# Kernel tuning notes

Measured on AMD Instinct MI355X. Metric: run time of the kernel, lower is better.

## Reference

```python
import jax, jax.numpy as jnp
import numpy as np

SEQ_LEN = 256
INPUT_DIM = 1
HIDDEN = 2048
CLASSES = 10
BATCH = 128


def setup_inputs() -> dict:
    key = jax.random.key(0)
    ks = jax.random.split(key, 6)
    x = jax.random.normal(ks[0], (BATCH, SEQ_LEN), dtype=jnp.float32)
    # Gate order along the 4H axis: g (cell candidate), i, f, o.
    Wx = jax.random.normal(ks[1], (INPUT_DIM, 4 * HIDDEN), dtype=jnp.float32) * 0.1
    Wh = jax.random.normal(ks[2], (HIDDEN, 4 * HIDDEN), dtype=jnp.float32) * (1.0 / np.sqrt(HIDDEN))
    b = jax.random.normal(ks[3], (4 * HIDDEN,), dtype=jnp.float32) * 0.1
    Wph = jax.random.normal(ks[4], (HIDDEN, CLASSES), dtype=jnp.float32) * (1.0 / np.sqrt(HIDDEN))
    bp = jax.random.normal(ks[5], (CLASSES,), dtype=jnp.float32) * 0.1
    return {"x": x, "Wx": Wx, "Wh": Wh, "b": b, "Wph": Wph, "bp": bp}


def reference(x, Wx, Wh, b, Wph, bp):
    B, T = x.shape
    H = Wh.shape[0]
    # Original loops over seq_length - 1 timesteps.
    xs = x[:, : T - 1].T[:, :, None]  # [T-1, B, 1]

    def step(carry, x_t):
        h, c = carry
        z = x_t @ Wx + h @ Wh + b  # [B, 4H] fused gate GEMM
        g = jnp.tanh(z[:, 0 * H:1 * H])
        i = jax.nn.sigmoid(z[:, 1 * H:2 * H])
        f = jax.nn.sigmoid(z[:, 2 * H:3 * H])
        o = jax.nn.sigmoid(z[:, 3 * H:4 * H])
        c = g * i + c * f
        h = jnp.tanh(c) * o
        return (h, c), None

    h0 = jnp.zeros((B, H), dtype=x.dtype)
    c0 = jnp.zeros((B, H), dtype=x.dtype)
    (h, _), _ = jax.lax.scan(step, (h0, c0), xs)
    logits = h @ Wph + bp
    return jax.nn.softmax(logits, axis=1)
```

## Files before the change

kernel.cpp:

```cpp
#include <hip/hip_runtime.h>
#include <hip/hip_bf16.h>

#define SEQ_LEN 256
#define HIDDEN  2048
#define CLASSES 10
#define BATCH   128
#define NWG     256
#define WG_THREADS 512
#define STEPS   (SEQ_LEN - 1)
#define KTILES  64
#define PF      16
#define LDS_WH  131072
#define LDS_ALL (LDS_WH + 4096)

typedef __attribute__((ext_vector_type(8))) short  bf16x8;
typedef __attribute__((ext_vector_type(8))) unsigned short u16x8;
typedef __attribute__((ext_vector_type(4))) float  f32x4;
typedef __attribute__((ext_vector_type(4))) unsigned int u32x4;

#define WHP_OFF  0
#define HB_OFF   33554432UL
#define HF_OFF   (HB_OFF + 4UL * 524288UL)
#define BAR_OFF  (HF_OFF + 1048576UL)

__device__ __forceinline__ unsigned short f2bf(float f) {
    unsigned int u = __float_as_uint(f);
    return (unsigned short)((u + 0x7FFFu + ((u >> 16) & 1u)) >> 16);
}
__device__ __forceinline__ float sigm(float z)  { return 1.0f / (1.0f + __expf(-z)); }
__device__ __forceinline__ float tanh_f(float z){ return 2.0f / (1.0f + __expf(-2.0f * z)) - 1.0f; }

__device__ __forceinline__ unsigned int aload(const unsigned int* p) {
    return __hip_atomic_load(p, __ATOMIC_RELAXED, __HIP_MEMORY_SCOPE_AGENT);
}
__device__ __forceinline__ void astore(unsigned int* p, unsigned int v) {
    __hip_atomic_store(p, v, __ATOMIC_RELAXED, __HIP_MEMORY_SCOPE_AGENT);
}

__global__ void lstm_pack_kernel(const float* __restrict__ Wh,
                                 unsigned short* __restrict__ whp,
                                 unsigned short* __restrict__ hbufs,
                                 unsigned int* __restrict__ bar) {
    int chunk = blockIdx.x * 256 + threadIdx.x;
    int lane = chunk & 63;
    int nt   = (chunk >> 6) & 1;
    int kt   = (chunk >> 7) & 63;
    int W    = chunk >> 13;
    int q = lane >> 4, l16 = lane & 15;
    int c32  = nt * 16 + l16;
    int gate = c32 >> 3, u = c32 & 7;
    int n    = gate * 2048 + W * 8 + u;
    int k0   = kt * 32 + q * 8;
    u16x8 frag;
    #pragma unroll
    for (int j = 0; j < 8; ++j)
        frag[j] = f2bf(Wh[(size_t)(k0 + j) * 8192 + n]);
    ((u16x8*)whp)[chunk] = frag;

    if (chunk < 32768) ((u32x4*)hbufs)[chunk] = (u32x4){0, 0, 0, 0};
    if (chunk < 2048) bar[chunk] = 0u;
}

__device__ __forceinline__ void grid_barrier(unsigned int* bar, unsigned int phase,
                                             bool do_inv, int W) {
    __syncthreads();
    if (threadIdx.x < 64) {
        const int lane = threadIdx.x;
        if (lane == 0) astore(&bar[W], phase);
        if (W < 8) {
            unsigned int* sl = &bar[W * 32 + (lane & 31)];
            while (!__all((int)(aload(sl) >= phase)))
                __builtin_amdgcn_s_sleep(1);
            if (lane == 0) astore(&bar[512 + 16 * W], phase);
            if (W == 0) {
                unsigned int* dn = &bar[512 + 16 * (lane & 7)];
                while (!__all((int)(aload(dn) >= phase)))
                    __builtin_amdgcn_s_sleep(1);
                if (lane < 32) astore(&bar[1024 + 16 * lane], phase);
            }
        }
        if (lane == 0 && W != 0) {
            unsigned int* rl = &bar[1024 + 16 * (W & 31)];
            while (aload(rl) < phase)
                __builtin_amdgcn_s_sleep(1);
        }
        if (do_inv)
            __builtin_amdgcn_fence(__ATOMIC_ACQUIRE, "agent");
    }
    __syncthreads();
}

__global__ __launch_bounds__(WG_THREADS, 2) void lstm_persist(
    const float* __restrict__ x,  const float* __restrict__ Wx,
    const float* __restrict__ b,  const float* __restrict__ Wph,
    const float* __restrict__ bp, const unsigned short* __restrict__ whp,
    unsigned short* hbufs, float* hfin,
    unsigned int* bar, float* out)
{
    extern __shared__ char lds[];
    const int tid = threadIdx.x;
    const int W   = blockIdx.x;

    {
        const u32x4* src = (const u32x4*)whp + (size_t)W * 8192;
        u32x4* dst = (u32x4*)lds;
        for (int i = tid; i < 8192; i += WG_THREADS) dst[i] = src[i];
    }
    unsigned short* hstage = (unsigned short*)(lds + LDS_WH);
    __syncthreads();

    const int lane = tid & 63;
    const int wv   = tid >> 6;
    const int q    = lane >> 4;
    const int l16  = lane & 15;
    const int s    = (lane >> 3) & 1;
    const int u    = lane & 7;
    const int rowA = wv * 16 + l16;
    const int row0 = wv * 16 + q * 4;
    const int colh = W * 8 + u;

    const int n0 = ((l16) >> 3) * 2048 + W * 8 + (l16 & 7);
    const int n1 = ((16 + l16) >> 3) * 2048 + W * 8 + ((16 + l16) & 7);
    const float wx0 = Wx[n0], bb0 = b[n0];
    const float wx1 = Wx[n1], bb1 = b[n1];

    const int abase = q * 128 + rowA;

    float c_state[4] = {0.f, 0.f, 0.f, 0.f};

    for (int t = 0; t < STEPS; ++t) {
        unsigned short* hcur  = hbufs + (size_t)(t & 3) * 262144;
        unsigned short* hnext = hbufs + (size_t)((t + 1) & 3) * 262144;

        const bf16x8* hc8 = (const bf16x8*)hcur;
        const char* lp = lds + lane * 16;

        float xv[4];
        #pragma unroll
        for (int r = 0; r < 4; ++r) xv[r] = x[(row0 + r) * SEQ_LEN + t];

        bf16x8 a_pf[PF];
        #pragma unroll
        for (int i = 0; i < PF; ++i)
            a_pf[i] = hc8[abase + i * 512];

        f32x4 acc0 = {0.f, 0.f, 0.f, 0.f};
        f32x4 acc1 = {0.f, 0.f, 0.f, 0.f};
        #pragma unroll 16
        for (int kt = 0; kt < KTILES - PF; ++kt) {
            bf16x8 a_cur = a_pf[kt & (PF - 1)];
            a_pf[kt & (PF - 1)] = hc8[abase + (kt + PF) * 512];
            bf16x8 b0 = *(const bf16x8*)(lp + (kt * 2 + 0) * 1024);
            bf16x8 b1 = *(const bf16x8*)(lp + (kt * 2 + 1) * 1024);
            acc0 = __builtin_amdgcn_mfma_f32_16x16x32_bf16(a_cur, b0, acc0, 0, 0, 0);
            acc1 = __builtin_amdgcn_mfma_f32_16x16x32_bf16(a_cur, b1, acc1, 0, 0, 0);
        }
        #pragma unroll
        for (int i = 0; i < PF; ++i) {
            const int kt = (KTILES - PF) + i;
            bf16x8 a_cur = a_pf[i];
            bf16x8 b0 = *(const bf16x8*)(lp + (kt * 2 + 0) * 1024);
            bf16x8 b1 = *(const bf16x8*)(lp + (kt * 2 + 1) * 1024);
            acc0 = __builtin_amdgcn_mfma_f32_16x16x32_bf16(a_cur, b0, acc0, 0, 0, 0);
            acc1 = __builtin_amdgcn_mfma_f32_16x16x32_bf16(a_cur, b1, acc1, 0, 0, 0);
        }

        const bool last = (t == STEPS - 1);
        #pragma unroll
        for (int r = 0; r < 4; ++r) {
            float z0 = acc0[r] + xv[r] * wx0 + bb0;
            float z1 = acc1[r] + xv[r] * wx1 + bb1;
            float p0 = __shfl_xor(z0, 8, 64);
            float p1 = __shfl_xor(z1, 8, 64);
            float zg = s ? p0 : z0;
            float zi = s ? z0 : p0;
            float zf = s ? p1 : z1;
            float zo = s ? z1 : p1;
            float cn = tanh_f(zg) * sigm(zi) + c_state[r] * sigm(zf);
            c_state[r] = cn;
            float h = tanh_f(cn) * sigm(zo);
            if (s == 0) {
                hstage[(row0 + r) * 8 + u] = f2bf(h);
                if (last)
                    __hip_atomic_store(&hfin[(row0 + r) * HIDDEN + colh], h,
                                       __ATOMIC_RELAXED, __HIP_MEMORY_SCOPE_AGENT);
            }
        }
        __syncthreads();
        astore(&((unsigned int*)hnext)[W * 512 + tid],
               ((const unsigned int*)hstage)[tid]);
        grid_barrier(bar, (unsigned int)(t + 1), (t & 3) == 2 || last, W);
    }

    if (W < BATCH) {
        float part[CLASSES];
        #pragma unroll
        for (int c = 0; c < CLASSES; ++c) part[c] = 0.f;
        for (int k = tid; k < HIDDEN; k += WG_THREADS) {
            float hv = hfin[W * HIDDEN + k];
            #pragma unroll
            for (int c = 0; c < CLASSES; ++c) part[c] += hv * Wph[k * CLASSES + c];
        }
        #pragma unroll
        for (int c = 0; c < CLASSES; ++c)
            for (int off = 32; off > 0; off >>= 1)
                part[c] += __shfl_xor(part[c], off, 64);
        float* red = (float*)(lds + LDS_WH);
        __syncthreads();
        if (lane == 0)
            for (int c = 0; c < CLASSES; ++c) red[wv * CLASSES + c] = part[c];
        __syncthreads();
        if (tid == 0) {
            float lg[CLASSES];
            for (int c = 0; c < CLASSES; ++c) {
                float sm = bp[c];
                for (int w8 = 0; w8 < 8; ++w8) sm += red[w8 * CLASSES + c];
                lg[c] = sm;
            }
            float mx = lg[0];
            for (int c = 1; c < CLASSES; ++c) mx = fmaxf(mx, lg[c]);
            float se = 0.f;
            for (int c = 0; c < CLASSES; ++c) { lg[c] = __expf(lg[c] - mx); se += lg[c]; }
            float inv = 1.0f / se;
            for (int c = 0; c < CLASSES; ++c) out[W * CLASSES + c] = lg[c] * inv;
        }
    }
}

extern "C" void kernel_launch(void* const* d_in, const int* in_sizes, int n_in,
                              void* d_out, int out_size, void* d_ws, size_t ws_size,
                              hipStream_t stream) {
    const float* x   = (const float*)d_in[0];
    const float* Wx  = (const float*)d_in[1];
    const float* Wh  = (const float*)d_in[2];
    const float* b   = (const float*)d_in[3];
    const float* Wph = (const float*)d_in[4];
    const float* bp  = (const float*)d_in[5];
    float* out = (float*)d_out;

    char* ws = (char*)d_ws;
    unsigned short* whp  = (unsigned short*)(ws + WHP_OFF);
    unsigned short* hbufs= (unsigned short*)(ws + HB_OFF);
    float*          hfin = (float*)(ws + HF_OFF);
    unsigned int*   bar  = (unsigned int*)(ws + BAR_OFF);

    hipFuncSetAttribute((const void*)lstm_persist,
                        hipFuncAttributeMaxDynamicSharedMemorySize, LDS_ALL);

    lstm_pack_kernel<<<8192, 256, 0, stream>>>(Wh, whp, hbufs, bar);
    lstm_persist<<<NWG, WG_THREADS, LDS_ALL, stream>>>(x, Wx, b, Wph, bp,
                                                       whp, hbufs, hfin, bar, out);
}
```

Measured before the change: 2.613 ms.

## Switch recurrent GEMM to 32x32x16 MFMA with split-K across wave pairs

Replaces the two 16x16x32 MFMAs per k-tile with one 32x32x16 MFMA covering 32 batch rows and all 32 gate columns. K is split in half between wave groups, and the partial sums are reduced through LDS. The Wh fragment packing is re-laid out to match, and gate values are gathered with three cross-lane shuffles. This halves LDS B-fragment reads per MFMA and uses the larger MFMA shape. In exchange it adds an LDS reduction and an extra barrier each step, and half the waves sit idle during the gate math.

```diff
diff --git a/kernel.cpp b/kernel.cpp
--- a/kernel.cpp
+++ b/kernel.cpp
@@ -11,12 +11,15 @@
 #define KTILES  64
 #define PF      16
 #define LDS_WH  131072
-#define LDS_ALL (LDS_WH + 4096)
-
-typedef __attribute__((ext_vector_type(8))) short  bf16x8;
-typedef __attribute__((ext_vector_type(8))) unsigned short u16x8;
-typedef __attribute__((ext_vector_type(4))) float  f32x4;
-typedef __attribute__((ext_vector_type(4))) unsigned int u32x4;
+#define RED_OFF    LDS_WH
+#define RED_STRIDE 72
+#define HSTAGE_OFF (LDS_WH + 18432)
+#define LDS_ALL    (HSTAGE_OFF + 2048)
+
+typedef __attribute__((ext_vector_type(8)))  short  bf16x8;
+typedef __attribute__((ext_vector_type(8)))  unsigned short u16x8;
+typedef __attribute__((ext_vector_type(16))) float  f32x16;
+typedef __attribute__((ext_vector_type(4)))  unsigned int u32x4;
 
 #define WHP_OFF  0
 #define HB_OFF   33554432UL
@@ -43,14 +46,14 @@
                                  unsigned int* __restrict__ bar) {
     int chunk = blockIdx.x * 256 + threadIdx.x;
     int lane = chunk & 63;
-    int nt   = (chunk >> 6) & 1;
-    int kt   = (chunk >> 7) & 63;
+    int kt   = (chunk >> 6) & 63;
+    int kh   = (chunk >> 12) & 1;
     int W    = chunk >> 13;
-    int q = lane >> 4, l16 = lane & 15;
-    int c32  = nt * 16 + l16;
-    int gate = c32 >> 3, u = c32 & 7;
+    int c    = lane & 31;
+    int oct  = lane >> 5;
+    int gate = c >> 3, u = c & 7;
     int n    = gate * 2048 + W * 8 + u;
-    int k0   = kt * 32 + q * 8;
+    int k0   = kh * 1024 + kt * 16 + oct * 8;
     u16x8 frag;
     #pragma unroll
     for (int j = 0; j < 8; ++j)
@@ -106,83 +109,109 @@
         u32x4* dst = (u32x4*)lds;
         for (int i = tid; i < 8192; i += WG_THREADS) dst[i] = src[i];
     }
-    unsigned short* hstage = (unsigned short*)(lds + LDS_WH);
+    unsigned short* hstage = (unsigned short*)(lds + HSTAGE_OFF);
     __syncthreads();
 
     const int lane = tid & 63;
     const int wv   = tid >> 6;
-    const int q    = lane >> 4;
-    const int l16  = lane & 15;
-    const int s    = (lane >> 3) & 1;
+    const int wv2  = wv & 3;
+    const int kh   = wv >> 2;
+    const int l31  = lane & 31;
+    const int oct  = lane >> 5;
     const int u    = lane & 7;
-    const int rowA = wv * 16 + l16;
-    const int row0 = wv * 16 + q * 4;
-    const int colh = W * 8 + u;
-
-    const int n0 = ((l16) >> 3) * 2048 + W * 8 + (l16 & 7);
-    const int n1 = ((16 + l16) >> 3) * 2048 + W * 8 + ((16 + l16) & 7);
-    const float wx0 = Wx[n0], bb0 = b[n0];
-    const float wx1 = Wx[n1], bb1 = b[n1];
-
-    const int abase = q * 128 + rowA;
-
+    const int gamma= (lane >> 3) & 3;
+
+    const int nbase = W * 8 + u;
+    float wxg[4], bbg[4];
+    #pragma unroll
+    for (int g = 0; g < 4; ++g) {
+        wxg[g] = Wx[g * 2048 + nbase];
+        bbg[g] = b[g * 2048 + nbase];
+    }
+
+    const int abase = kh * 16384 + oct * 128 + 32 * wv2 + l31;
+    const char* lpB0 = lds + kh * 65536 + lane * 16;
+
+    char* redp = lds + RED_OFF + (size_t)(wv2 * 64 + lane) * RED_STRIDE;
+
+    const int g0 = gamma & 1, g1 = (gamma >> 1) & 1;
     float c_state[4] = {0.f, 0.f, 0.f, 0.f};
 
     for (int t = 0; t < STEPS; ++t) {
         unsigned short* hcur  = hbufs + (size_t)(t & 3) * 262144;
         unsigned short* hnext = hbufs + (size_t)((t + 1) & 3) * 262144;
-
         const bf16x8* hc8 = (const bf16x8*)hcur;
-        const char* lp = lds + lane * 16;
-
-        float xv[4];
-        #pragma unroll
-        for (int r = 0; r < 4; ++r) xv[r] = x[(row0 + r) * SEQ_LEN + t];
+
+        float xva[4];
+        if (kh == 0) {
+            #pragma unroll
+            for (int a = 0; a < 4; ++a) {
+                int row = 32 * wv2 + gamma + 8 * a + 4 * oct;
+                xva[a] = x[row * SEQ_LEN + t];
+            }
+        }
 
         bf16x8 a_pf[PF];
         #pragma unroll
         for (int i = 0; i < PF; ++i)
-            a_pf[i] = hc8[abase + i * 512];
-
-        f32x4 acc0 = {0.f, 0.f, 0.f, 0.f};
-        f32x4 acc1 = {0.f, 0.f, 0.f, 0.f};
+            a_pf[i] = hc8[abase + i * 256];
+
+        f32x16 acc = {0.f};
         #pragma unroll 16
         for (int kt = 0; kt < KTILES - PF; ++kt) {
             bf16x8 a_cur = a_pf[kt & (PF - 1)];
-            a_pf[kt & (PF - 1)] = hc8[abase + (kt + PF) * 512];
-            bf16x8 b0 = *(const bf16x8*)(lp + (kt * 2 + 0) * 1024);
-            bf16x8 b1 = *(const bf16x8*)(lp + (kt * 2 + 1) * 1024);
-            acc0 = __builtin_amdgcn_mfma_f32_16x16x32_bf16(a_cur, b0, acc0, 0, 0, 0);
-            acc1 = __builtin_amdgcn_mfma_f32_16x16x32_bf16(a_cur, b1, acc1, 0, 0, 0);
+            a_pf[kt & (PF - 1)] = hc8[abase + (kt + PF) * 256];
+            bf16x8 bb = *(const bf16x8*)(lpB0 + kt * 1024);
+            acc = __builtin_amdgcn_mfma_f32_32x32x16_bf16(a_cur, bb, acc, 0, 0, 0);
         }
         #pragma unroll
         for (int i = 0; i < PF; ++i) {
-            const int kt = (KTILES - PF) + i;
-            bf16x8 a_cur = a_pf[i];
-            bf16x8 b0 = *(const bf16x8*)(lp + (kt * 2 + 0) * 1024);
-            bf16x8 b1 = *(const bf16x8*)(lp + (kt * 2 + 1) * 1024);
-            acc0 = __builtin_amdgcn_mfma_f32_16x16x32_bf16(a_cur, b0, acc0, 0, 0, 0);
-            acc1 = __builtin_amdgcn_mfma_f32_16x16x32_bf16(a_cur, b1, acc1, 0, 0, 0);
-        }
+            bf16x8 bb = *(const bf16x8*)(lpB0 + ((KTILES - PF) + i) * 1024);
+            acc = __builtin_amdgcn_mfma_f32_32x32x16_bf16(a_pf[i], bb, acc, 0, 0, 0);
+        }
+
+        if (kh == 1) {
+            #pragma unroll
+            for (int j = 0; j < 8; ++j) {
+                float2 v; v.x = acc[2 * j]; v.y = acc[2 * j + 1];
+                *(float2*)(redp + 8 * j) = v;
+            }
+        }
+        __syncthreads();
 
         const bool last = (t == STEPS - 1);
-        #pragma unroll
-        for (int r = 0; r < 4; ++r) {
-            float z0 = acc0[r] + xv[r] * wx0 + bb0;
-            float z1 = acc1[r] + xv[r] * wx1 + bb1;
-            float p0 = __shfl_xor(z0, 8, 64);
-            float p1 = __shfl_xor(z1, 8, 64);
-            float zg = s ? p0 : z0;
-            float zi = s ? z0 : p0;
-            float zf = s ? p1 : z1;
-            float zo = s ? z1 : p1;
-            float cn = tanh_f(zg) * sigm(zi) + c_state[r] * sigm(zf);
-            c_state[r] = cn;
-            float h = tanh_f(cn) * sigm(zo);
-            if (s == 0) {
-                hstage[(row0 + r) * 8 + u] = f2bf(h);
+        if (kh == 0) {
+            #pragma unroll
+            for (int j = 0; j < 8; ++j) {
+                float2 v = *(const float2*)(redp + 8 * j);
+                acc[2 * j] += v.x; acc[2 * j + 1] += v.y;
+            }
+            #pragma unroll
+            for (int a = 0; a < 4; ++a) {
+                float q0 = acc[4 * a + 0], q1 = acc[4 * a + 1];
+                float q2 = acc[4 * a + 2], q3 = acc[4 * a + 3];
+                float s1  = g0 ? (g1 ? q2 : q0) : (g1 ? q3 : q1);
+                float s2  = g1 ? (g0 ? q1 : q0) : (g0 ? q3 : q2);
+                float s3  = g1 ? (g0 ? q0 : q1) : (g0 ? q2 : q3);
+                float own = g1 ? (g0 ? q3 : q2) : (g0 ? q1 : q0);
+                float r1 = __shfl_xor(s1, 8, 64);
+                float r2 = __shfl_xor(s2, 16, 64);
+                float r3 = __shfl_xor(s3, 24, 64);
+                float zg = g1 ? (g0 ? r3 : r2) : (g0 ? r1 : own);
+                float zi = g1 ? (g0 ? r2 : r3) : (g0 ? own : r1);
+                float zf = g1 ? (g0 ? r1 : own) : (g0 ? r3 : r2);
+                float zo = g1 ? (g0 ? own : r1) : (g0 ? r2 : r3);
+                zg += xva[a] * wxg[0] + bbg[0];
+                zi += xva[a] * wxg[1] + bbg[1];
+                zf += xva[a] * wxg[2] + bbg[2];
+                zo += xva[a] * wxg[3] + bbg[3];
+                float cn = tanh_f(zg) * sigm(zi) + c_state[a] * sigm(zf);
+                c_state[a] = cn;
+                float h = tanh_f(cn) * sigm(zo);
+                int row = 32 * wv2 + gamma + 8 * a + 4 * oct;
+                hstage[row * 8 + u] = f2bf(h);
                 if (last)
-                    __hip_atomic_store(&hfin[(row0 + r) * HIDDEN + colh], h,
+                    __hip_atomic_store(&hfin[row * HIDDEN + W * 8 + u], h,
                                        __ATOMIC_RELAXED, __HIP_MEMORY_SCOPE_AGENT);
             }
         }
@@ -207,8 +236,9 @@
                 part[c] += __shfl_xor(part[c], off, 64);
         float* red = (float*)(lds + LDS_WH);
         __syncthreads();
-        if (lane == 0)
-            for (int c = 0; c < CLASSES; ++c) red[wv * CLASSES + c] = part[c];
+        const int wvq = tid >> 6;
+        if ((tid & 63) == 0)
+            for (int c = 0; c < CLASSES; ++c) red[wvq * CLASSES + c] = part[c];
         __syncthreads();
         if (tid == 0) {
             float lg[CLASSES];
```

After: 2.442 ms. 1.07x faster.
